# Kernel tuning notes

Hardware: AMD Instinct MI355X
Metric: run time of the kernel (lower is better)

Reference implementation:

```python
import jax, jax.numpy as jnp
import numpy as np

MARGIN = 0.3

def setup_inputs() -> dict:
    key = jax.random.key(0)
    k1, k2 = jax.random.split(key)
    embeddings = jax.random.normal(k1, (8192, 512), dtype=jnp.float32)
    labels = jax.random.randint(k2, (8192,), 0, 128, dtype=jnp.int64)
    return {"embeddings": embeddings, "labels": labels}

def _pairwise_euclidean(x):
    # ||xi - xj|| via GEMM, matching torch reference (relu clamp + sqrt(.+1e-16))
    dot = x @ x.T                      # [B, B]
    sq = jnp.diagonal(dot)             # [B]
    d2 = sq[None, :] - 2.0 * dot + sq[:, None]
    d2 = jnp.maximum(d2, 0.0)
    return jnp.sqrt(d2 + 1e-16)

def reference(embeddings, labels):
    n = embeddings.shape[0]
    d = _pairwise_euclidean(embeddings)                 # [B, B]
    same = labels[:, None] == labels[None, :]           # [B, B]
    eye = jnp.eye(n, dtype=bool)
    mask_pos = same & ~eye
    mask_neg = ~same
    # fused masked row-wise reductions (hard mining)
    hardest_pos = jnp.max(jnp.where(mask_pos, d, -jnp.inf), axis=1)  # [B]
    hardest_neg = jnp.min(jnp.where(mask_neg, d, jnp.inf), axis=1)   # [B]
    valid = mask_pos.any(axis=1) & mask_neg.any(axis=1)              # [B]
    per_row = jax.nn.relu(hardest_pos - hardest_neg + MARGIN)
    per_row = jnp.where(valid, per_row, 0.0)
    denom = jnp.maximum(jnp.sum(valid.astype(per_row.dtype)), 1.0)
    return jnp.sum(per_row) / denom
```

## Files before the change

### kernel.cpp

```cpp
#include <hip/hip_runtime.h>

#define BATCH 8192
#define DIM   512

typedef __attribute__((ext_vector_type(4))) float  f32x4;
typedef __attribute__((ext_vector_type(8))) __bf16 bf16x8;

__device__ __forceinline__ unsigned short f2bf(float x) {
  unsigned u = __float_as_uint(x);
  u = (u + 0x7FFFu + ((u >> 16) & 1u)) >> 16;
  return (unsigned short)u;
}

__device__ __forceinline__ void load_lds16(const void* g, void* l) {
  __builtin_amdgcn_global_load_lds(
      (__attribute__((address_space(1))) void*)(g),
      (__attribute__((address_space(3))) void*)(l), 16, 0, 0);
}

__device__ __forceinline__ unsigned enc(float f) {
  unsigned u = __float_as_uint(f);
  return u ^ (unsigned)(((int)u >> 31) | 0x80000000);
}
__device__ __forceinline__ float dec(unsigned k) {
  unsigned u = (k & 0x80000000u) ? (k ^ 0x80000000u) : ~k;
  return __uint_as_float(u);
}

__global__ __launch_bounds__(256) void prep_kernel(
    const float* __restrict__ X, unsigned short* __restrict__ Xb,
    float* __restrict__ sq, float* __restrict__ ctrl) {
  if (blockIdx.x == 0 && threadIdx.x == 0) {
    ctrl[0] = 0.f; ctrl[1] = 0.f;
    ((unsigned*)ctrl)[2] = 0u;
  }
  int wave = threadIdx.x >> 6, lane = threadIdx.x & 63;
  int row = blockIdx.x * 4 + wave;
  const float4* xr = (const float4*)(X + (size_t)row * DIM);
  float4 a = xr[lane * 2];
  float4 b = xr[lane * 2 + 1];
  float s = a.x*a.x + a.y*a.y + a.z*a.z + a.w*a.w
          + b.x*b.x + b.y*b.y + b.z*b.z + b.w*b.w;
  uint4 p;
  p.x = (unsigned)f2bf(a.x) | ((unsigned)f2bf(a.y) << 16);
  p.y = (unsigned)f2bf(a.z) | ((unsigned)f2bf(a.w) << 16);
  p.z = (unsigned)f2bf(b.x) | ((unsigned)f2bf(b.y) << 16);
  p.w = (unsigned)f2bf(b.z) | ((unsigned)f2bf(b.w) << 16);
  ((uint4*)(Xb + (size_t)row * DIM))[lane] = p;
  #pragma unroll
  for (int off = 32; off > 0; off >>= 1) s += __shfl_down(s, off);
  if (lane == 0) sq[row] = s;
}

template<bool STRAD>
__device__ __forceinline__ void epilogue(
    const f32x4 (&acc)[4][8], const float* __restrict__ sq,
    const int* __restrict__ labels,
    int i0, int jwin, int wm, int wn, int quad, int lc,
    unsigned (*ibuf)[128][2], unsigned (*jbuf)[256][2]) {
  float sqj_r[8]; int labj_r[8];
  #pragma unroll
  for (int ni = 0; ni < 8; ni++) {
    int j = jwin + wn * 128 + ni * 16 + lc;
    sqj_r[ni] = sq[j]; labj_r[ni] = labels[j];
  }
  float rpos[16], rneg[16];
  float jp[8], jn[8];
  #pragma unroll
  for (int x = 0; x < 8; x++) { jp[x] = -3e38f; jn[x] = 3e38f; }
  #pragma unroll
  for (int mi = 0; mi < 4; mi++) {
    #pragma unroll
    for (int r = 0; r < 4; r++) {
      int ig = i0 + wm * 64 + mi * 16 + quad * 4 + r;
      int li = labels[ig];
      float si = sq[ig];
      float rp = -3e38f, rn = 3e38f;
      #pragma unroll
      for (int ni = 0; ni < 8; ni++) {
        float a = acc[mi][ni][r];
        float v = fmaf(-2.f, a, sqj_r[ni]);
        bool same = (li == labj_r[ni]);
        bool posok = same;
        if (STRAD) posok = same && ((jwin + wn * 128 + ni * 16 + lc) != ig);
        rp = fmaxf(rp, posok ? v : -3e38f);
        rn = fminf(rn, same ? 3e38f : v);
        if (!STRAD) {
          float v2 = fmaf(-2.f, a, si);
          jp[ni] = fmaxf(jp[ni], same ? v2 : -3e38f);
          jn[ni] = fminf(jn[ni], same ? 3e38f : v2);
        }
      }
      rpos[mi * 4 + r] = rp; rneg[mi * 4 + r] = rn;
    }
  }
  #pragma unroll
  for (int m = 1; m <= 8; m <<= 1)
    #pragma unroll
    for (int x = 0; x < 16; x++) {
      rpos[x] = fmaxf(rpos[x], __shfl_xor(rpos[x], m));
      rneg[x] = fminf(rneg[x], __shfl_xor(rneg[x], m));
    }
  if (lc == 0) {
    #pragma unroll
    for (int mi = 0; mi < 4; mi++)
      #pragma unroll
      for (int r = 0; r < 4; r++) {
        int row = wm * 64 + mi * 16 + quad * 4 + r;
        ibuf[wn][row][0] = enc(rpos[mi * 4 + r]);
        ibuf[wn][row][1] = enc(rneg[mi * 4 + r]);
      }
  }
  if (!STRAD) {
    #pragma unroll
    for (int m = 16; m <= 32; m <<= 1)
      #pragma unroll
      for (int x = 0; x < 8; x++) {
        jp[x] = fmaxf(jp[x], __shfl_xor(jp[x], m));
        jn[x] = fminf(jn[x], __shfl_xor(jn[x], m));
      }
    if (quad == 0) {
      #pragma unroll
      for (int ni = 0; ni < 8; ni++) {
        int col = wn * 128 + ni * 16 + lc;
        jbuf[wm][col][0] = enc(jp[ni]);
        jbuf[wm][col][1] = enc(jn[ni]);
      }
    }
  }
}

__global__ __launch_bounds__(256, 2) void triplet_mfma(
    const unsigned short* __restrict__ Xb, const float* __restrict__ sq,
    const int* __restrict__ labels,
    unsigned* __restrict__ pos_i, unsigned* __restrict__ neg_i,
    unsigned* __restrict__ pos_j, unsigned* __restrict__ neg_j) {
  __shared__ __align__(16) unsigned short Asm[128 * 64];
  __shared__ __align__(16) unsigned short Bsm[256 * 64];
  __shared__ unsigned ibuf[2][128][2];
  __shared__ unsigned jbuf[2][256][2];

  int tid = threadIdx.x, bid = blockIdx.x;
  int wave = tid >> 6, lane = tid & 63;
  int wm = wave >> 1, wn = wave & 1;
  int quad = lane >> 4, lc = lane & 15;
  int rc = lane >> 3;
  int gcol = ((lane & 7) ^ rc) * 8;

  int start = (bid * 33) >> 4, end = ((bid + 1) * 33) >> 4;
  for (int t = start; t < end; ++t) {
    int It, Js; bool strad;
    if (t < 64) { It = t; Js = t >> 1; strad = true; }
    else {
      int u = t - 64; It = 0; Js = 0;
      for (int s = 0; s < 64; s++) {
        int c = 31 - (s >> 1);
        if (u < c) { It = s; Js = (s >> 1) + 1 + u; break; }
        u -= c;
      }
      strad = false;
    }
    int i0 = It * 128, jwin = Js * 256;

    f32x4 acc[4][8];
    #pragma unroll
    for (int mi = 0; mi < 4; mi++)
      #pragma unroll
      for (int ni = 0; ni < 8; ni++)
        acc[mi][ni] = (f32x4){0.f, 0.f, 0.f, 0.f};

    for (int k0 = 0; k0 < DIM; k0 += 64) {
      #pragma unroll
      for (int tt = 0; tt < 4; tt++) {
        int c = wave * 4 + tt;
        int row = c * 8 + rc;
        load_lds16(Xb + (size_t)(i0 + row) * DIM + k0 + gcol, &Asm[c * 512]);
      }
      #pragma unroll
      for (int tt = 0; tt < 8; tt++) {
        int c = wave * 8 + tt;
        int row = c * 8 + rc;
        load_lds16(Xb + (size_t)(jwin + row) * DIM + k0 + gcol, &Bsm[c * 512]);
      }
      __syncthreads();
      #pragma unroll
      for (int kk = 0; kk < 64; kk += 32) {
        int kc = kk >> 3;
        int asel = ((kc + quad) ^ (lc & 7)) * 8;
        bf16x8 af[4], bfr[8];
        #pragma unroll
        for (int mi = 0; mi < 4; mi++)
          af[mi] = *(const bf16x8*)&Asm[(wm * 64 + mi * 16 + lc) * 64 + asel];
        #pragma unroll
        for (int ni = 0; ni < 8; ni++)
          bfr[ni] = *(const bf16x8*)&Bsm[(wn * 128 + ni * 16 + lc) * 64 + asel];
        #pragma unroll
        for (int mi = 0; mi < 4; mi++)
          #pragma unroll
          for (int ni = 0; ni < 8; ni++)
            acc[mi][ni] = __builtin_amdgcn_mfma_f32_16x16x32_bf16(
                af[mi], bfr[ni], acc[mi][ni], 0, 0, 0);
      }
      __syncthreads();
    }

    if (strad)
      epilogue<true >(acc, sq, labels, i0, jwin, wm, wn, quad, lc, ibuf, jbuf);
    else
      epilogue<false>(acc, sq, labels, i0, jwin, wm, wn, quad, lc, ibuf, jbuf);
    __syncthreads();

    if (tid < 128) {
      unsigned p = max(ibuf[0][tid][0], ibuf[1][tid][0]);
      unsigned n = min(ibuf[0][tid][1], ibuf[1][tid][1]);
      pos_i[(size_t)Js * BATCH + i0 + tid] = p;
      neg_i[(size_t)Js * BATCH + i0 + tid] = n;
    }
    if (!strad) {
      unsigned p = max(jbuf[0][tid][0], jbuf[1][tid][0]);
      unsigned n = min(jbuf[0][tid][1], jbuf[1][tid][1]);
      pos_j[(size_t)It * BATCH + jwin + tid] = p;
      neg_j[(size_t)It * BATCH + jwin + tid] = n;
    }
  }
}

__global__ __launch_bounds__(256) void final_kernel(
    const unsigned* __restrict__ pos_i, const unsigned* __restrict__ neg_i,
    const unsigned* __restrict__ pos_j, const unsigned* __restrict__ neg_j,
    const float* __restrict__ sq, float* __restrict__ ctrl,
    float* __restrict__ out) {
  int i = blockIdx.x * 256 + threadIdx.x;
  unsigned pe = 0u, ne = 0xFFFFFFFFu;
  #pragma unroll 4
  for (int s = 0; s < 32; s++) {
    pe = max(pe, pos_i[(size_t)s * BATCH + i]);
    ne = min(ne, neg_i[(size_t)s * BATCH + i]);
  }
  #pragma unroll 4
  for (int s = 0; s < 64; s++) {
    pe = max(pe, pos_j[(size_t)s * BATCH + i]);
    ne = min(ne, neg_j[(size_t)s * BATCH + i]);
  }
  float p = dec(pe), n = dec(ne);
  float term = 0.f, cnt = 0.f;
  if (p > -1e37f && n < 1e37f) {
    float si = sq[i];
    float dp = sqrtf(fmaxf(si + p, 0.f) + 1e-16f);
    float dn = sqrtf(fmaxf(si + n, 0.f) + 1e-16f);
    term = fmaxf(dp - dn + 0.3f, 0.f);
    cnt = 1.f;
  }
  #pragma unroll
  for (int off = 32; off > 0; off >>= 1) {
    term += __shfl_down(term, off);
    cnt  += __shfl_down(cnt, off);
  }
  __shared__ float ss[4], sc[4];
  int wave = threadIdx.x >> 6, lane = threadIdx.x & 63;
  if (lane == 0) { ss[wave] = term; sc[wave] = cnt; }
  __syncthreads();
  if (threadIdx.x == 0) {
    atomicAdd(&ctrl[0], ss[0] + ss[1] + ss[2] + ss[3]);
    atomicAdd(&ctrl[1], sc[0] + sc[1] + sc[2] + sc[3]);
    __threadfence();
    unsigned t = atomicAdd((unsigned*)&ctrl[2], 1u);
    if (t == 31u) {
      float S = atomicAdd(&ctrl[0], 0.f);
      float C = atomicAdd(&ctrl[1], 0.f);
      out[0] = S / fmaxf(C, 1.f);
    }
  }
}

extern "C" void kernel_launch(void* const* d_in, const int* in_sizes, int n_in,
                              void* d_out, int out_size, void* d_ws, size_t ws_size,
                              hipStream_t stream) {
  const float* X      = (const float*)d_in[0];
  const int*   labels = (const int*)d_in[1];
  float* out = (float*)d_out;
  char* ws = (char*)d_ws;

  const size_t SLOT = (size_t)BATCH * 4;
  unsigned short* Xb = (unsigned short*)ws;
  float* sq   = (float*)(ws + (8u << 20));
  float* ctrl = (float*)(ws + (8u << 20) + (32u << 10));
  char*  posb = ws + (8u << 20) + (64u << 10);
  char*  negb = posb + 96 * SLOT;
  unsigned* pos_i = (unsigned*)posb;
  unsigned* pos_j = (unsigned*)(posb + 32 * SLOT);
  unsigned* neg_i = (unsigned*)negb;
  unsigned* neg_j = (unsigned*)(negb + 32 * SLOT);

  hipMemsetAsync(posb, 0x00, 96 * SLOT, stream);
  hipMemsetAsync(negb, 0xFF, 96 * SLOT, stream);
  prep_kernel<<<BATCH / 4, 256, 0, stream>>>(X, Xb, sq, ctrl);
  triplet_mfma<<<512, 256, 0, stream>>>(Xb, sq, labels, pos_i, neg_i, pos_j, neg_j);
  final_kernel<<<BATCH / 256, 256, 0, stream>>>(pos_i, neg_i, pos_j, neg_j, sq, ctrl, out);
}
```

Before: 148.7 us.

## Use atomic work-stealing tile scheduler and fold buffer init into prep kernel

Replaces the static per-block tile ranges with a dynamic scheduler: each block claims tiles through an atomic counter in the ctrl buffer until all 1056 tiles are taken. Tile costs differ (straddling diagonal tiles versus full off-diagonal ones), so this aims to balance load across blocks. The two hipMemsetAsync calls are removed and the pos/neg partial buffers are now initialized inside prep_kernel, cutting two launches. The cost is one atomic plus an extra barrier per tile.

```diff
diff --git a/kernel.cpp b/kernel.cpp
--- a/kernel.cpp
+++ b/kernel.cpp
@@ -2,6 +2,7 @@
 
 #define BATCH 8192
 #define DIM   512
+#define NTILE 1056
 
 typedef __attribute__((ext_vector_type(4))) float  f32x4;
 typedef __attribute__((ext_vector_type(8))) __bf16 bf16x8;
@@ -29,10 +30,17 @@
 
 __global__ __launch_bounds__(256) void prep_kernel(
     const float* __restrict__ X, unsigned short* __restrict__ Xb,
-    float* __restrict__ sq, float* __restrict__ ctrl) {
-  if (blockIdx.x == 0 && threadIdx.x == 0) {
+    float* __restrict__ sq, float* __restrict__ ctrl,
+    uint4* __restrict__ pos4, uint4* __restrict__ neg4) {
+  int gid = blockIdx.x * 256 + threadIdx.x;
+  if (gid == 0) {
     ctrl[0] = 0.f; ctrl[1] = 0.f;
     ((unsigned*)ctrl)[2] = 0u;
+    ((unsigned*)ctrl)[3] = 0u;
+  }
+  if (gid < 196608) {
+    pos4[gid] = (uint4){0u, 0u, 0u, 0u};
+    neg4[gid] = (uint4){~0u, ~0u, ~0u, ~0u};
   }
   int wave = threadIdx.x >> 6, lane = threadIdx.x & 63;
   int row = blockIdx.x * 4 + wave;
@@ -132,33 +140,37 @@
 
 __global__ __launch_bounds__(256, 2) void triplet_mfma(
     const unsigned short* __restrict__ Xb, const float* __restrict__ sq,
-    const int* __restrict__ labels,
+    const int* __restrict__ labels, float* __restrict__ ctrl,
     unsigned* __restrict__ pos_i, unsigned* __restrict__ neg_i,
     unsigned* __restrict__ pos_j, unsigned* __restrict__ neg_j) {
   __shared__ __align__(16) unsigned short Asm[128 * 64];
   __shared__ __align__(16) unsigned short Bsm[256 * 64];
   __shared__ unsigned ibuf[2][128][2];
   __shared__ unsigned jbuf[2][256][2];
-
-  int tid = threadIdx.x, bid = blockIdx.x;
+  __shared__ int tshare;
+
+  int tid = threadIdx.x;
   int wave = tid >> 6, lane = tid & 63;
   int wm = wave >> 1, wn = wave & 1;
   int quad = lane >> 4, lc = lane & 15;
   int rc = lane >> 3;
   int gcol = ((lane & 7) ^ rc) * 8;
 
-  int start = (bid * 33) >> 4, end = ((bid + 1) * 33) >> 4;
-  for (int t = start; t < end; ++t) {
+  for (;;) {
+    if (tid == 0) tshare = (int)atomicAdd((unsigned*)ctrl + 3, 1u);
+    __syncthreads();
+    int t = tshare;
+    if (t >= NTILE) break;
+
     int It, Js; bool strad;
     if (t < 64) { It = t; Js = t >> 1; strad = true; }
     else {
-      int u = t - 64; It = 0; Js = 0;
+      int u = t - 64; It = 0; Js = 0; strad = false;
       for (int s = 0; s < 64; s++) {
         int c = 31 - (s >> 1);
         if (u < c) { It = s; Js = (s >> 1) + 1 + u; break; }
         u -= c;
       }
-      strad = false;
     }
     int i0 = It * 128, jwin = Js * 256;
 
@@ -222,6 +234,7 @@
       pos_j[(size_t)It * BATCH + jwin + tid] = p;
       neg_j[(size_t)It * BATCH + jwin + tid] = n;
     }
+    __syncthreads();
   }
 }
 
@@ -292,9 +305,9 @@
   unsigned* neg_i = (unsigned*)negb;
   unsigned* neg_j = (unsigned*)(negb + 32 * SLOT);
 
-  hipMemsetAsync(posb, 0x00, 96 * SLOT, stream);
-  hipMemsetAsync(negb, 0xFF, 96 * SLOT, stream);
-  prep_kernel<<<BATCH / 4, 256, 0, stream>>>(X, Xb, sq, ctrl);
-  triplet_mfma<<<512, 256, 0, stream>>>(Xb, sq, labels, pos_i, neg_i, pos_j, neg_j);
+  prep_kernel<<<BATCH / 4, 256, 0, stream>>>(X, Xb, sq, ctrl,
+                                             (uint4*)posb, (uint4*)negb);
+  triplet_mfma<<<512, 256, 0, stream>>>(Xb, sq, labels, ctrl,
+                                        pos_i, neg_i, pos_j, neg_j);
   final_kernel<<<BATCH / 256, 256, 0, stream>>>(pos_i, neg_i, pos_j, neg_j, sq, ctrl, out);
 }
```

Result: faster. 138.0 us (-7.2%).
